# Performance work log

Measured on AMD Instinct MI355X. Metric: run time of the kernel, lower is better.

The kernel has to match this reference:

```python
import jax, jax.numpy as jnp
import numpy as np

HID = 2048
NH = 16
HD = HID // NH  # 128
EPS = 1e-6
BASE = 10000.0


def _rmsnorm(x, w):
    xf = x.astype(jnp.float32)
    y = xf * jax.lax.rsqrt(jnp.mean(xf * xf, axis=-1, keepdims=True) + EPS)
    return y.astype(x.dtype) * w


def _rope_cos_sin(seq_len, dtype):
    inv_freq = 1.0 / (BASE ** (jnp.arange(0, HD, 2, dtype=jnp.float32) / HD))
    t = jnp.arange(seq_len, dtype=jnp.float32)
    freqs = jnp.outer(t, inv_freq)          # [S, HD/2]
    emb = jnp.concatenate([freqs, freqs], axis=-1)  # [S, HD]
    return jnp.cos(emb).astype(dtype), jnp.sin(emb).astype(dtype)


def _rotate_half(x):
    x1, x2 = jnp.split(x, 2, axis=-1)
    return jnp.concatenate([-x2, x1], axis=-1)


def setup_inputs() -> dict:
    key = jax.random.key(0)
    ks = jax.random.split(key, 8)
    B, S = 2, 2048
    s = 0.02
    return {
        "hidden_states": jax.random.normal(ks[0], (B, S, HID), jnp.float32),
        "Wq": jax.random.normal(ks[1], (HID, HID), jnp.float32) * s,
        "Wk": jax.random.normal(ks[2], (HID, HID), jnp.float32) * s,
        "Wv": jax.random.normal(ks[3], (HID, HID), jnp.float32) * s,
        "Wo": jax.random.normal(ks[4], (HID, HID), jnp.float32) * s,
        "w1": jax.random.normal(ks[5], (HID, HID), jnp.float32) * s,
        "w2": jax.random.normal(ks[6], (HID, HID), jnp.float32) * s,
        "w3": jax.random.normal(ks[7], (HID, HID), jnp.float32) * s,
        "ln1_w": jnp.ones((HID,), jnp.float32),
        "ln2_w": jnp.ones((HID,), jnp.float32),
    }


def reference(hidden_states, Wq, Wk, Wv, Wo, w1, w2, w3, ln1_w, ln2_w):
    B, S, _ = hidden_states.shape
    residual = hidden_states
    x = _rmsnorm(hidden_states, ln1_w)

    # projections -> [B, NH, S, HD]
    q = (x @ Wq).reshape(B, S, NH, HD).transpose(0, 2, 1, 3)
    k = (x @ Wk).reshape(B, S, NH, HD).transpose(0, 2, 1, 3)
    v = (x @ Wv).reshape(B, S, NH, HD).transpose(0, 2, 1, 3)

    cos, sin = _rope_cos_sin(S, x.dtype)  # [S, HD]
    cos = cos[None, None]  # broadcast over batch and heads
    sin = sin[None, None]
    q = q * cos + _rotate_half(q) * sin
    k = k * cos + _rotate_half(k) * sin

    scores = jnp.einsum("bhqd,bhkd->bhqk", q, k) / np.sqrt(HD).astype(np.float32)
    # no attention_mask (torch default path). fp32 softmax.
    attn = jax.nn.softmax(scores.astype(jnp.float32), axis=-1).astype(q.dtype)
    ctx = jnp.einsum("bhqk,bhkd->bhqd", attn, v)  # [B, NH, S, HD]
    ctx = ctx.transpose(0, 2, 1, 3).reshape(B, S, HID)
    attn_out = ctx @ Wo

    h = residual + attn_out
    residual = h
    y = _rmsnorm(h, ln2_w)
    mlp = (jax.nn.silu(y @ w1) * (y @ w3)) @ w2
    return residual + mlp
```

## Files before the change

### kernel.cpp

```cpp
#include <hip/hip_runtime.h>

#define HIDN 2048
#define NHEAD 16
#define HD 128
#define SEQ 2048
#define BATCH 2
#define NROWS (BATCH*SEQ)

typedef __bf16 bf16_t;
typedef bf16_t bf16x8 __attribute__((ext_vector_type(8)));
typedef float f32x4 __attribute__((ext_vector_type(4)));

#define AS1 __attribute__((address_space(1)))
#define AS3 __attribute__((address_space(3)))

__device__ __forceinline__ unsigned short f2bf(float x) {
  union { bf16_t b; unsigned short u; } cv; cv.b = (bf16_t)x; return cv.u;
}

#define MFMA16(a,b,c) __builtin_amdgcn_mfma_f32_16x16x32_bf16((a),(b),(c),0,0,0)

__device__ __forceinline__ void gload16(const void* g, void* l) {
  __builtin_amdgcn_global_load_lds((const AS1 void*)g, (AS3 void*)l, 16, 0, 0);
}

__global__ __launch_bounds__(256) void transpose_all_kernel(
    const float* __restrict__ Wq, const float* __restrict__ Wk,
    const float* __restrict__ Wv, const float* __restrict__ Wo,
    const float* __restrict__ w1, const float* __restrict__ w3,
    const float* __restrict__ w2, unsigned short* __restrict__ wblk) {
  const int z = blockIdx.z;
  const float* W; unsigned short* dstb; int tmode = 0, half = 0;
  switch (z) {
    case 0: W = Wq; dstb = wblk;                       tmode = 1; break;
    case 1: W = Wk; dstb = wblk + (size_t)2048 * HIDN; tmode = 1; break;
    case 2: W = Wv; dstb = wblk + (size_t)4096 * HIDN; break;
    case 3: W = Wo; dstb = wblk + (size_t)6144 * HIDN; break;
    case 4: W = w1; dstb = wblk + (size_t)8192 * HIDN; tmode = 2; half = 0; break;
    case 5: W = w3; dstb = wblk + (size_t)8192 * HIDN; tmode = 2; half = 1; break;
    default: W = w2; dstb = wblk + (size_t)12288 * HIDN; break;
  }
  __shared__ float t[64][69];
  const int tid = threadIdx.x;
  const int bn = blockIdx.x * 64, bk = blockIdx.y * 64;
  const int lc = (tid & 15) * 4, lrw = tid >> 4;
#pragma unroll
  for (int i = 0; i < 4; ++i) {
    int k = bk + lrw + i * 16;
    float4 v = *(const float4*)(W + (long)k * HIDN + bn + lc);
    t[lrw + i * 16][lc] = v.x; t[lrw + i * 16][lc + 1] = v.y;
    t[lrw + i * 16][lc + 2] = v.z; t[lrw + i * 16][lc + 3] = v.w;
  }
  __syncthreads();
  const int nl = tid >> 2, k0 = (tid & 3) * 16;
  int n = bn + nl;
  int dst;
  if (tmode == 0) dst = n;
  else if (tmode == 1) { int d = n & 127; dst = (n & ~127) | ((d & 63) << 1) | (d >> 6); }
  else dst = (n >> 4) * 32 + half * 16 + (n & 15);
  unsigned short* orow = dstb + (long)dst * HIDN + bk + k0;
#pragma unroll
  for (int j = 0; j < 16; j += 4) {
    ushort4 o;
    o.x = f2bf(t[k0 + j][nl]);     o.y = f2bf(t[k0 + j + 1][nl]);
    o.z = f2bf(t[k0 + j + 2][nl]); o.w = f2bf(t[k0 + j + 3][nl]);
    *(ushort4*)(orow + j) = o;
  }
}

__global__ void rope_table_kernel(float* __restrict__ cosT, float* __restrict__ sinT) {
  int s = blockIdx.x, d = threadIdx.x;
  float invf = powf(10000.0f, (-2.0f * (float)d) / 128.0f);
  float ang = (float)s * invf;
  cosT[s * 64 + d] = cosf(ang);
  sinT[s * 64 + d] = sinf(ang);
}

__global__ __launch_bounds__(256) void rmsnorm_kernel(
    const float* __restrict__ x, const float* __restrict__ w, unsigned short* __restrict__ out) {
  long row = blockIdx.x;
  const float* xr = x + row * HIDN;
  int c0 = threadIdx.x * 4;
  float4 v0 = *(const float4*)(xr + c0);
  float4 v1 = *(const float4*)(xr + 1024 + c0);
  float s = v0.x*v0.x + v0.y*v0.y + v0.z*v0.z + v0.w*v0.w
          + v1.x*v1.x + v1.y*v1.y + v1.z*v1.z + v1.w*v1.w;
#pragma unroll
  for (int off = 1; off < 64; off <<= 1) s += __shfl_xor(s, off);
  __shared__ float red[4];
  if ((threadIdx.x & 63) == 0) red[threadIdx.x >> 6] = s;
  __syncthreads();
  float tot = red[0] + red[1] + red[2] + red[3];
  float r = 1.0f / sqrtf(tot * (1.0f / (float)HIDN) + 1e-6f);
  float4 w0 = *(const float4*)(w + c0);
  float4 w1 = *(const float4*)(w + 1024 + c0);
  ushort4 o0, o1;
  o0.x = f2bf(v0.x * r * w0.x); o0.y = f2bf(v0.y * r * w0.y);
  o0.z = f2bf(v0.z * r * w0.z); o0.w = f2bf(v0.w * r * w0.w);
  o1.x = f2bf(v1.x * r * w1.x); o1.y = f2bf(v1.y * r * w1.y);
  o1.z = f2bf(v1.z * r * w1.z); o1.w = f2bf(v1.w * r * w1.w);
  *(ushort4*)(out + row * HIDN + c0) = o0;
  *(ushort4*)(out + row * HIDN + 1024 + c0) = o1;
}

template <int MODE>
__global__ __launch_bounds__(512, 2) void gemm256_kernel(
    const unsigned short* __restrict__ A, const unsigned short* __restrict__ Bt,
    int nbx,
    void* __restrict__ p0, void* __restrict__ p1, void* __restrict__ p2,
    const float* __restrict__ cosT, const float* __restrict__ sinT) {
  __shared__ unsigned short L[65536];
  const int tid = threadIdx.x;
  const int wave = tid >> 6, lane = tid & 63;
  const int lr = lane & 15, lkg = lane >> 4;
  const int wr = wave >> 2, wc = wave & 3;
  const int x7 = lr & 7;
  const int nwg = (int)gridDim.x;
  const int bid = (int)blockIdx.x;
  const int wg = (bid & 7) * (nwg >> 3) + (bid >> 3);
  const int bx = wg % nbx, by = wg / nbx;
  const long bm = (long)by * 256, bn = (long)bx * 256;
  const int sslot = (lane & 7) ^ (lane >> 3);
  const unsigned short* Ag = A + (bm + wave * 8 + (lane >> 3)) * HIDN + sslot * 8;
  const unsigned short* Bg = Bt + (bn + wave * 8 + (lane >> 3)) * HIDN + sslot * 8;
  const char* Lc = (const char*)L;
  f32x4 acc[8][4] = {};
  bf16x8 af[2][2], bfr[4][2];

#define STG(b, mat, half, tile)                                                   \
  {                                                                               \
    const unsigned short* gsrc = ((mat) ? Bg : Ag) + ((long)(half) * 128) * HIDN + (long)(tile) * 64; \
    unsigned short* ldst = &L[((4 * (b) + 2 * (mat) + (half)) * 8192) + wave * 8 * 64]; \
    gload16(gsrc, ldst);                                                          \
    gload16(gsrc + (long)64 * HIDN, ldst + 4096);                                 \
  }
#define DSRA(b, q)                                                                \
  { _Pragma("unroll") for (int mm = 0; mm < 2; ++mm) {                            \
      int row128 = ((q) * 2 + mm) * 16 + lr;                                      \
      _Pragma("unroll") for (int ks = 0; ks < 2; ++ks) {                          \
        int s = ks * 4 + lkg;                                                     \
        af[mm][ks] = *(const bf16x8*)(Lc + (4 * (b) + wr) * 16384 + row128 * 128 + ((s ^ x7) << 4)); \
      } } }
#define DSRB(b)                                                                   \
  { _Pragma("unroll") for (int n = 0; n < 4; ++n) {                               \
      int row128 = (wc & 1) * 64 + n * 16 + lr;                                   \
      _Pragma("unroll") for (int ks = 0; ks < 2; ++ks) {                          \
        int s = ks * 4 + lkg;                                                     \
        bfr[n][ks] = *(const bf16x8*)(Lc + (4 * (b) + 2 + (wc >> 1)) * 16384 + row128 * 128 + ((s ^ x7) << 4)); \
      } } }
#define MFMAQ(q)                                                                  \
  { __builtin_amdgcn_s_setprio(1);                                                \
    _Pragma("unroll") for (int mm = 0; mm < 2; ++mm)                              \
      _Pragma("unroll") for (int n = 0; n < 4; ++n) {                             \
        acc[(q) * 2 + mm][n] = MFMA16(af[mm][0], bfr[n][0], acc[(q) * 2 + mm][n]); \
        acc[(q) * 2 + mm][n] = MFMA16(af[mm][1], bfr[n][1], acc[(q) * 2 + mm][n]); \
      }                                                                           \
    __builtin_amdgcn_s_setprio(0); }
#define BARR __builtin_amdgcn_s_barrier()
#define LGK0 { asm volatile("s_waitcnt lgkmcnt(0)" ::: "memory"); __builtin_amdgcn_sched_barrier(0); }

  STG(0, 0, 0, 0); STG(0, 0, 1, 0); STG(0, 1, 0, 0); STG(0, 1, 1, 0);
  STG(1, 1, 0, 1); STG(1, 1, 1, 1); STG(1, 0, 0, 1);
  asm volatile("s_waitcnt vmcnt(6)" ::: "memory");
  __builtin_amdgcn_sched_barrier(0);
  BARR;

  const int NIT = HIDN / 128;
#pragma unroll 1
  for (int i = 0; i < NIT; ++i) {
    const int t2 = 2 * i + 2, t3 = 2 * i + 3;
    const bool nl_ = (i < NIT - 1);
    DSRA(0, 0); DSRB(0);
    STG(1, 0, 1, 2 * i + 1);
    asm volatile("s_waitcnt lgkmcnt(8)" ::: "memory");
    BARR; LGK0; MFMAQ(0); BARR;
    DSRA(0, 1);
    if (nl_) STG(0, 1, 0, t2);
    BARR; LGK0; MFMAQ(1); BARR;
    DSRA(0, 2);
    if (nl_) STG(0, 1, 1, t2);
    BARR; LGK0; MFMAQ(2); BARR;
    DSRA(0, 3);
    BARR; LGK0; MFMAQ(3);
    if (nl_) { asm volatile("s_waitcnt vmcnt(4)" ::: "memory"); }
    else     { asm volatile("s_waitcnt vmcnt(0)" ::: "memory"); }
    __builtin_amdgcn_sched_barrier(0);
    BARR;
    DSRA(1, 0); DSRB(1);
    if (nl_) STG(0, 0, 0, t2);
    asm volatile("s_waitcnt lgkmcnt(8)" ::: "memory");
    BARR; LGK0; MFMAQ(0); BARR;
    DSRA(1, 1);
    if (nl_) { STG(0, 0, 1, t2); STG(1, 1, 0, t3); }
    BARR; LGK0; MFMAQ(1); BARR;
    DSRA(1, 2);
    if (nl_) STG(1, 1, 1, t3);
    BARR; LGK0; MFMAQ(2); BARR;
    DSRA(1, 3);
    if (nl_) STG(1, 0, 0, t3);
    BARR; LGK0; MFMAQ(3);
    if (nl_) { asm volatile("s_waitcnt vmcnt(6)" ::: "memory"); __builtin_amdgcn_sched_barrier(0); }
    BARR;
  }
#undef STG
#undef DSRA
#undef DSRB
#undef MFMAQ
#undef BARR
#undef LGK0

  const int gc0 = (int)bn + wc * 64;
  if (MODE == 1) {
    unsigned short* bout = (unsigned short*)p0;
#pragma unroll
    for (int m = 0; m < 8; ++m) {
      long r0 = bm + wr * 128 + m * 16 + lkg * 4;
#pragma unroll
      for (int n = 0; n < 4; n += 2) {
        int ggrp = (gc0 + n * 16) >> 5;
        long c = (long)ggrp * 16 + lr;
#pragma unroll
        for (int r = 0; r < 4; ++r) {
          float x = acc[m][n][r], g = acc[m][n + 1][r];
          float sv = x / (1.0f + __expf(-x)) * g;
          bout[(r0 + r) * 2048 + c] = f2bf(sv);
        }
      }
    }
  } else {
    int bufid = gc0 >> 11;
    if (bufid == 2) {
      unsigned short* vT = (unsigned short*)p2;
#pragma unroll
      for (int m = 0; m < 8; ++m) {
        long r0 = bm + wr * 128 + m * 16 + lkg * 4;
        long bq = r0 >> 11;
        int s = (int)(r0 & 2047);
#pragma unroll
        for (int n = 0; n < 4; ++n) {
          int wcol = (gc0 + n * 16 + lr) & 2047;
          int hh = wcol >> 7, dd = wcol & 127;
          ushort4 pw;
          pw.x = f2bf(acc[m][n][0]); pw.y = f2bf(acc[m][n][1]);
          pw.z = f2bf(acc[m][n][2]); pw.w = f2bf(acc[m][n][3]);
          *(ushort4*)(vT + ((bq * 16 + hh) * 128 + dd) * (long)SEQ + s) = pw;
        }
      }
    } else {
      unsigned short* dst = (bufid == 0) ? (unsigned short*)p0 : (unsigned short*)p1;
      const float qscale = (bufid == 0) ? 0.12751689f : 1.0f;
#pragma unroll
      for (int m = 0; m < 8; ++m) {
        long r0 = bm + wr * 128 + m * 16 + lkg * 4;
#pragma unroll
        for (int n = 0; n < 4; ++n) {
          int wcol = (gc0 + n * 16 + lr) & 2047;
          int f = wcol & 127, hh = wcol >> 7;
          int j = f >> 1, odd = f & 1;
          int oc = hh * 128 + (odd ? 64 : 0) + j;
#pragma unroll
          for (int r = 0; r < 4; ++r) {
            long row = r0 + r;
            int s = (int)(row & (SEQ - 1));
            float cv = cosT[s * 64 + j], sn = sinT[s * 64 + j];
            float v = acc[m][n][r];
            float o = __shfl_xor(v, 1);
            float res = (odd ? (v * cv + o * sn) : (v * cv - o * sn)) * qscale;
            dst[row * 2048 + oc] = f2bf(res);
          }
        }
      }
    }
  }
}

template <int MODE>
__global__ __launch_bounds__(256) void gemm_kernel(
    const unsigned short* __restrict__ A, const unsigned short* __restrict__ Bt, int N,
    void* __restrict__ p0, const void* __restrict__ p1) {
  __shared__ unsigned short As[128 * 32];
  __shared__ unsigned short Bs[128 * 32];
  const int tid = threadIdx.x;
  const int lane = tid & 63, wave = tid >> 6;
  const int wm = (wave >> 1) * 64, wn = (wave & 1) * 64;
  const int lr = lane & 15, lkg = lane >> 4;
  const long bm = (long)blockIdx.y * 128, bn = (long)blockIdx.x * 128;
  f32x4 acc[4][4] = {};
  const int rA0 = wave * 32 + (lane >> 2);
  const int gs0 = (lane & 3) ^ ((rA0 >> 1) & 3);
  const int gs1 = (lane & 3) ^ (((rA0 + 16) >> 1) & 3);
  const unsigned short* Ag0 = A + (bm + rA0) * HIDN + gs0 * 8;
  const unsigned short* Ag1 = A + (bm + rA0 + 16) * HIDN + gs1 * 8;
  const unsigned short* Bg0 = Bt + (bn + rA0) * HIDN + gs0 * 8;
  const unsigned short* Bg1 = Bt + (bn + rA0 + 16) * HIDN + gs1 * 8;
  unsigned short* lA0 = &As[(wave * 32) * 32];
  unsigned short* lA1 = &As[(wave * 32 + 16) * 32];
  unsigned short* lB0 = &Bs[(wave * 32) * 32];
  unsigned short* lB1 = &Bs[(wave * 32 + 16) * 32];
  for (int k0 = 0; k0 < HIDN; k0 += 32) {
    __syncthreads();
    gload16(Ag0 + k0, lA0);
    gload16(Ag1 + k0, lA1);
    gload16(Bg0 + k0, lB0);
    gload16(Bg1 + k0, lB1);
    __syncthreads();
    bf16x8 af[4], bfr[4];
#pragma unroll
    for (int m = 0; m < 4; ++m) {
      int row = wm + m * 16 + lr;
      af[m] = *(const bf16x8*)((const char*)As + row * 64 + ((lkg ^ ((row >> 1) & 3)) << 4));
    }
#pragma unroll
    for (int n = 0; n < 4; ++n) {
      int row = wn + n * 16 + lr;
      bfr[n] = *(const bf16x8*)((const char*)Bs + row * 64 + ((lkg ^ ((row >> 1) & 3)) << 4));
    }
#pragma unroll
    for (int m = 0; m < 4; ++m)
#pragma unroll
      for (int n = 0; n < 4; ++n) acc[m][n] = MFMA16(af[m], bfr[n], acc[m][n]);
  }
  float* fout = (float*)p0;
  const float* addsrc = (const float*)p1;
#pragma unroll
  for (int m = 0; m < 4; ++m)
#pragma unroll
    for (int n = 0; n < 4; ++n) {
      long r0 = bm + wm + m * 16 + lkg * 4;
      long c = bn + wn + n * 16 + lr;
#pragma unroll
      for (int r = 0; r < 4; ++r) {
        long idx = (r0 + r) * 2048 + c;
        if (MODE == 2) fout[idx] = addsrc[idx] + acc[m][n][r];
        else fout[idx] = fout[idx] + acc[m][n][r];
      }
    }
}

__global__ __launch_bounds__(256, 3) void flash_attn_kernel(
    const unsigned short* __restrict__ Q, const unsigned short* __restrict__ Kb,
    const unsigned short* __restrict__ vT, unsigned short* __restrict__ O) {
  __shared__ unsigned short Ks[64 * 128];
  __shared__ unsigned short Vs[128 * 64];
  __shared__ unsigned short Ps[4][16][72];
  const int bid = (int)blockIdx.x;
  const int wg = (bid & 7) * 128 + (bid >> 3);
  const int qt = wg & 31, h = (wg >> 5) & 15, b = wg >> 9;
  const int tid = threadIdx.x, wave = tid >> 6, lane = tid & 63;
  const int lr = lane & 15, lkg = lane >> 4, lk = lkg * 8;
  const long rowbase = (long)b * SEQ;
  const int qrow0 = qt * 64 + wave * 16;
  bf16x8 aq[4];
#pragma unroll
  for (int ks = 0; ks < 4; ++ks)
    aq[ks] = *(const bf16x8*)(Q + (rowbase + qrow0 + lr) * HIDN + h * HD + ks * 32 + lk);
  const unsigned short* vbase = vT + ((long)(b * 16 + h) * 128) * SEQ;
  const int kr_ = tid >> 4, kc_ = tid & 15;
  const int vd_ = tid >> 3, vc_ = tid & 7;
  int4 kreg[4], vreg[4];
  f32x4 acc[8] = {};
  float m_ = -3.0e38f, l_ = 0.f;

#define GLOADKV(kv0_)                                                              \
  { _Pragma("unroll")                                                              \
    for (int j = 0; j < 4; ++j)                                                    \
      kreg[j] = *(const int4*)(Kb + (rowbase + (kv0_) + kr_ + j * 16) * HIDN + h * HD + kc_ * 8); \
    _Pragma("unroll")                                                              \
    for (int j = 0; j < 4; ++j)                                                    \
      vreg[j] = *(const int4*)(vbase + (long)(vd_ + j * 32) * SEQ + (kv0_) + vc_ * 8); }
#define DSWRITEKV()                                                                \
  { _Pragma("unroll")                                                              \
    for (int j = 0; j < 4; ++j) {                                                  \
      int row = kr_ + j * 16;                                                      \
      *(int4*)((char*)Ks + row * 256 + ((kc_ ^ (row & 15)) << 4)) = kreg[j];       \
    }                                                                              \
    _Pragma("unroll")                                                              \
    for (int j = 0; j < 4; ++j) {                                                  \
      int d = vd_ + j * 32;                                                        \
      *(int4*)((char*)Vs + d * 128 + ((vc_ ^ (d & 7)) << 4)) = vreg[j];            \
    } }

  GLOADKV(0);
  asm volatile("s_waitcnt vmcnt(0)" ::: "memory");
  DSWRITEKV();
  asm volatile("s_waitcnt lgkmcnt(0)" ::: "memory");
  __builtin_amdgcn_sched_barrier(0);
  asm volatile("s_barrier" ::: "memory");

  for (int t = 0; t < SEQ / 64; ++t) {
    if (t + 1 < SEQ / 64) GLOADKV((long)(t + 1) * 64);
    const char* ksb = (const char*)Ks;
    f32x4 sa[4] = {};
#pragma unroll
    for (int n = 0; n < 4; ++n) {
      int row = n * 16 + lr;
#pragma unroll
      for (int ks = 0; ks < 4; ++ks) {
        bf16x8 bk = *(const bf16x8*)(ksb + row * 256 + (((ks * 4 + lkg) ^ (row & 15)) << 4));
        sa[n] = MFMA16(bk, aq[ks], sa[n]);
      }
    }
    float pmax = sa[0][0];
#pragma unroll
    for (int n = 0; n < 4; ++n)
#pragma unroll
      for (int r = 0; r < 4; ++r) pmax = fmaxf(pmax, sa[n][r]);
    pmax = fmaxf(pmax, __shfl_xor(pmax, 16));
    pmax = fmaxf(pmax, __shfl_xor(pmax, 32));
    if (__all(pmax - m_ <= 11.54f)) {
      float psum = 0.f;
#pragma unroll
      for (int n = 0; n < 4; ++n)
#pragma unroll
        for (int r = 0; r < 4; ++r) {
          float p = exp2f(sa[n][r] - m_);
          sa[n][r] = p;
          psum += p;
        }
      psum += __shfl_xor(psum, 16);
      psum += __shfl_xor(psum, 32);
      l_ += psum;
    } else {
      float mnew = fmaxf(m_, pmax);
      float corr = exp2f(m_ - mnew);
      float psum = 0.f;
#pragma unroll
      for (int n = 0; n < 4; ++n)
#pragma unroll
        for (int r = 0; r < 4; ++r) {
          float p = exp2f(sa[n][r] - mnew);
          sa[n][r] = p;
          psum += p;
        }
      psum += __shfl_xor(psum, 16);
      psum += __shfl_xor(psum, 32);
      l_ = l_ * corr + psum;
      m_ = mnew;
      float corr4[4];
#pragma unroll
      for (int r = 0; r < 4; ++r) corr4[r] = __shfl(corr, 4 * lkg + r);
#pragma unroll
      for (int df = 0; df < 8; ++df)
#pragma unroll
        for (int r = 0; r < 4; ++r) acc[df][r] *= corr4[r];
    }
#pragma unroll
    for (int n = 0; n < 4; ++n) {
      ushort4 pw;
      pw.x = f2bf(sa[n][0]); pw.y = f2bf(sa[n][1]);
      pw.z = f2bf(sa[n][2]); pw.w = f2bf(sa[n][3]);
      *(ushort4*)&Ps[wave][lr][n * 16 + 4 * lkg] = pw;
    }
    bf16x8 pa0 = *(const bf16x8*)&Ps[wave][lr][lk];
    bf16x8 pa1 = *(const bf16x8*)&Ps[wave][lr][32 + lk];
    const char* vsb = (const char*)Vs;
#pragma unroll
    for (int df = 0; df < 8; ++df) {
      int row = df * 16 + lr;
      int x7 = row & 7;
      bf16x8 bv0 = *(const bf16x8*)(vsb + row * 128 + ((lkg ^ x7) << 4));
      bf16x8 bv1 = *(const bf16x8*)(vsb + row * 128 + (((4 + lkg) ^ x7) << 4));
      acc[df] = MFMA16(pa0, bv0, acc[df]);
      acc[df] = MFMA16(pa1, bv1, acc[df]);
    }
    asm volatile("s_barrier" ::: "memory");
    if (t + 1 < SEQ / 64) {
      asm volatile("s_waitcnt vmcnt(0)" ::: "memory");
      DSWRITEKV();
      asm volatile("s_waitcnt lgkmcnt(0)" ::: "memory");
      __builtin_amdgcn_sched_barrier(0);
      asm volatile("s_barrier" ::: "memory");
    }
  }
#undef GLOADKV
#undef DSWRITEKV
  float invl = 1.0f / l_;
  float invl4[4];
#pragma unroll
  for (int r = 0; r < 4; ++r) invl4[r] = __shfl(invl, 4 * lkg + r);
#pragma unroll
  for (int r = 0; r < 4; ++r) {
    long orow = rowbase + qrow0 + lkg * 4 + r;
#pragma unroll
    for (int df = 0; df < 8; ++df)
      O[orow * HIDN + h * HD + df * 16 + lr] = f2bf(acc[df][r] * invl4[r]);
  }
}

extern "C" void kernel_launch(void* const* d_in, const int* in_sizes, int n_in,
                              void* d_out, int out_size, void* d_ws, size_t ws_size,
                              hipStream_t stream) {
  const float* hidden = (const float*)d_in[0];
  const float* Wq = (const float*)d_in[1];
  const float* Wk = (const float*)d_in[2];
  const float* Wv = (const float*)d_in[3];
  const float* Wo = (const float*)d_in[4];
  const float* w1 = (const float*)d_in[5];
  const float* w2 = (const float*)d_in[6];
  const float* w3 = (const float*)d_in[7];
  const float* ln1 = (const float*)d_in[8];
  const float* ln2 = (const float*)d_in[9];
  float* out = (float*)d_out;

  char* ws = (char*)d_ws;
  size_t off = 0;
  auto alloc = [&](size_t bytes) -> void* {
    void* p = ws + off;
    off += (bytes + 255) & ~(size_t)255;
    return p;
  };
  unsigned short* wblk = (unsigned short*)alloc((size_t)(2048L * 6 + 2048) * HIDN * 2);
  unsigned short* wQ = wblk;
  unsigned short* wG = wblk + (size_t)8192 * HIDN;
  unsigned short* wO = wblk + (size_t)6144 * HIDN;
  unsigned short* wD = wblk + (size_t)12288 * HIDN;
  unsigned short* xb   = (unsigned short*)alloc((size_t)NROWS * HIDN * 2);
  unsigned short* qb   = (unsigned short*)alloc((size_t)NROWS * HIDN * 2);
  unsigned short* kb   = (unsigned short*)alloc((size_t)NROWS * HIDN * 2);
  unsigned short* vTb  = (unsigned short*)alloc((size_t)NROWS * HIDN * 2);
  unsigned short* ctxb = (unsigned short*)alloc((size_t)NROWS * HIDN * 2);
  float* cosT = (float*)alloc((size_t)SEQ * 64 * 4);
  float* sinT = (float*)alloc((size_t)SEQ * 64 * 4);
  if (off > ws_size) return;

  transpose_all_kernel<<<dim3(HIDN / 64, HIDN / 64, 7), 256, 0, stream>>>(
      Wq, Wk, Wv, Wo, w1, w3, w2, wblk);
  rope_table_kernel<<<SEQ, 64, 0, stream>>>(cosT, sinT);

  rmsnorm_kernel<<<NROWS, 256, 0, stream>>>(hidden, ln1, xb);

  gemm256_kernel<0><<<(6144 / 256) * (NROWS / 256), 512, 0, stream>>>(
      xb, wQ, 6144 / 256, qb, kb, vTb, cosT, sinT);

  flash_attn_kernel<<<(SEQ / 64) * NHEAD * BATCH, 256, 0, stream>>>(qb, kb, vTb, ctxb);

  gemm_kernel<2><<<dim3(2048 / 128, NROWS / 128), 256, 0, stream>>>(
      ctxb, wO, 2048, out, hidden);

  rmsnorm_kernel<<<NROWS, 256, 0, stream>>>(out, ln2, xb);

  gemm256_kernel<1><<<(4096 / 256) * (NROWS / 256), 512, 0, stream>>>(
      xb, wG, 4096 / 256, qb, nullptr, nullptr, nullptr, nullptr);

  gemm_kernel<3><<<dim3(2048 / 128, NROWS / 128), 256, 0, stream>>>(
      qb, wD, 2048, out, nullptr);
}
```

Before: 463.6 us.

## Switch flash attention to 32x32 MFMA with 128-row query tiles

Flash attention now uses 32x32x16 bf16 MFMA and gives each wave 32 query rows, so a block covers 128 queries instead of 64. Each K/V tile loaded into shared memory is reused across twice as many queries, which halves K/V global traffic and LDS staging per query. The softmax reductions and output layout are rewritten for the 32x32 accumulator. In exchange the block count halves (to 512), register pressure rises, and launch bounds drop to two blocks per CU.

```diff
diff --git a/kernel.cpp b/kernel.cpp
--- a/kernel.cpp
+++ b/kernel.cpp
@@ -10,6 +10,7 @@
 typedef __bf16 bf16_t;
 typedef bf16_t bf16x8 __attribute__((ext_vector_type(8)));
 typedef float f32x4 __attribute__((ext_vector_type(4)));
+typedef float f32x16 __attribute__((ext_vector_type(16)));
 
 #define AS1 __attribute__((address_space(1)))
 #define AS3 __attribute__((address_space(3)))
@@ -19,6 +20,7 @@
 }
 
 #define MFMA16(a,b,c) __builtin_amdgcn_mfma_f32_16x16x32_bf16((a),(b),(c),0,0,0)
+#define MFMA32(a,b,c) __builtin_amdgcn_mfma_f32_32x32x16_bf16((a),(b),(c),0,0,0)
 
 __device__ __forceinline__ void gload16(const void* g, void* l) {
   __builtin_amdgcn_global_load_lds((const AS1 void*)g, (AS3 void*)l, 16, 0, 0);
@@ -337,28 +339,28 @@
     }
 }
 
-__global__ __launch_bounds__(256, 3) void flash_attn_kernel(
+__global__ __launch_bounds__(256, 2) void flash_attn_kernel(
     const unsigned short* __restrict__ Q, const unsigned short* __restrict__ Kb,
     const unsigned short* __restrict__ vT, unsigned short* __restrict__ O) {
   __shared__ unsigned short Ks[64 * 128];
   __shared__ unsigned short Vs[128 * 64];
-  __shared__ unsigned short Ps[4][16][72];
+  __shared__ unsigned short Ps[4][32][72];
   const int bid = (int)blockIdx.x;
-  const int wg = (bid & 7) * 128 + (bid >> 3);
-  const int qt = wg & 31, h = (wg >> 5) & 15, b = wg >> 9;
+  const int wg = (bid & 7) * 64 + (bid >> 3);
+  const int qt = wg & 15, h = (wg >> 4) & 15, b = wg >> 8;
   const int tid = threadIdx.x, wave = tid >> 6, lane = tid & 63;
-  const int lr = lane & 15, lkg = lane >> 4, lk = lkg * 8;
+  const int l31 = lane & 31, hi = lane >> 5;
   const long rowbase = (long)b * SEQ;
-  const int qrow0 = qt * 64 + wave * 16;
-  bf16x8 aq[4];
-#pragma unroll
-  for (int ks = 0; ks < 4; ++ks)
-    aq[ks] = *(const bf16x8*)(Q + (rowbase + qrow0 + lr) * HIDN + h * HD + ks * 32 + lk);
+  const int qrow0 = qt * 128 + wave * 32;
+  bf16x8 aq[8];
+#pragma unroll
+  for (int ds = 0; ds < 8; ++ds)
+    aq[ds] = *(const bf16x8*)(Q + (rowbase + qrow0 + l31) * HIDN + h * HD + ds * 16 + 8 * hi);
   const unsigned short* vbase = vT + ((long)(b * 16 + h) * 128) * SEQ;
   const int kr_ = tid >> 4, kc_ = tid & 15;
   const int vd_ = tid >> 3, vc_ = tid & 7;
   int4 kreg[4], vreg[4];
-  f32x4 acc[8] = {};
+  f32x16 acc[4] = {};
   float m_ = -3.0e38f, l_ = 0.f;
 
 #define GLOADKV(kv0_)                                                              \
@@ -390,78 +392,79 @@
   for (int t = 0; t < SEQ / 64; ++t) {
     if (t + 1 < SEQ / 64) GLOADKV((long)(t + 1) * 64);
     const char* ksb = (const char*)Ks;
-    f32x4 sa[4] = {};
-#pragma unroll
-    for (int n = 0; n < 4; ++n) {
-      int row = n * 16 + lr;
-#pragma unroll
-      for (int ks = 0; ks < 4; ++ks) {
-        bf16x8 bk = *(const bf16x8*)(ksb + row * 256 + (((ks * 4 + lkg) ^ (row & 15)) << 4));
-        sa[n] = MFMA16(bk, aq[ks], sa[n]);
-      }
-    }
-    float pmax = sa[0][0];
-#pragma unroll
-    for (int n = 0; n < 4; ++n)
-#pragma unroll
-      for (int r = 0; r < 4; ++r) pmax = fmaxf(pmax, sa[n][r]);
-    pmax = fmaxf(pmax, __shfl_xor(pmax, 16));
-    pmax = fmaxf(pmax, __shfl_xor(pmax, 32));
+    f32x16 sa0 = {}, sa1 = {};
+#pragma unroll
+    for (int ds = 0; ds < 8; ++ds) {
+      int c16 = 2 * ds + hi;
+      int r0 = l31;
+      int r1 = 32 + l31;
+      bf16x8 k0 = *(const bf16x8*)(ksb + r0 * 256 + ((c16 ^ (r0 & 15)) << 4));
+      bf16x8 k1 = *(const bf16x8*)(ksb + r1 * 256 + ((c16 ^ (r1 & 15)) << 4));
+      sa0 = MFMA32(k0, aq[ds], sa0);
+      sa1 = MFMA32(k1, aq[ds], sa1);
+    }
+    float mx[16];
+#pragma unroll
+    for (int i = 0; i < 16; ++i) mx[i] = fmaxf(sa0[i], sa1[i]);
+#pragma unroll
+    for (int s = 8; s > 0; s >>= 1)
+#pragma unroll
+      for (int i = 0; i < 8; ++i) if (i < s) mx[i] = fmaxf(mx[i], mx[i + s]);
+    float pmax = fmaxf(mx[0], __shfl_xor(mx[0], 32));
     if (__all(pmax - m_ <= 11.54f)) {
-      float psum = 0.f;
-#pragma unroll
-      for (int n = 0; n < 4; ++n)
-#pragma unroll
-        for (int r = 0; r < 4; ++r) {
-          float p = exp2f(sa[n][r] - m_);
-          sa[n][r] = p;
-          psum += p;
-        }
-      psum += __shfl_xor(psum, 16);
-      psum += __shfl_xor(psum, 32);
-      l_ += psum;
+      float ps[16];
+#pragma unroll
+      for (int i = 0; i < 16; ++i) {
+        float p0 = exp2f(sa0[i] - m_), p1 = exp2f(sa1[i] - m_);
+        sa0[i] = p0; sa1[i] = p1; ps[i] = p0 + p1;
+      }
+#pragma unroll
+      for (int s = 8; s > 0; s >>= 1)
+#pragma unroll
+        for (int i = 0; i < 8; ++i) if (i < s) ps[i] += ps[i + s];
+      l_ += ps[0] + __shfl_xor(ps[0], 32);
     } else {
       float mnew = fmaxf(m_, pmax);
       float corr = exp2f(m_ - mnew);
-      float psum = 0.f;
-#pragma unroll
-      for (int n = 0; n < 4; ++n)
-#pragma unroll
-        for (int r = 0; r < 4; ++r) {
-          float p = exp2f(sa[n][r] - mnew);
-          sa[n][r] = p;
-          psum += p;
-        }
-      psum += __shfl_xor(psum, 16);
-      psum += __shfl_xor(psum, 32);
-      l_ = l_ * corr + psum;
+      float ps[16];
+#pragma unroll
+      for (int i = 0; i < 16; ++i) {
+        float p0 = exp2f(sa0[i] - mnew), p1 = exp2f(sa1[i] - mnew);
+        sa0[i] = p0; sa1[i] = p1; ps[i] = p0 + p1;
+      }
+#pragma unroll
+      for (int s = 8; s > 0; s >>= 1)
+#pragma unroll
+        for (int i = 0; i < 8; ++i) if (i < s) ps[i] += ps[i + s];
+      l_ = l_ * corr + ps[0] + __shfl_xor(ps[0], 32);
       m_ = mnew;
-      float corr4[4];
-#pragma unroll
-      for (int r = 0; r < 4; ++r) corr4[r] = __shfl(corr, 4 * lkg + r);
-#pragma unroll
-      for (int df = 0; df < 8; ++df)
-#pragma unroll
-        for (int r = 0; r < 4; ++r) acc[df][r] *= corr4[r];
-    }
-#pragma unroll
-    for (int n = 0; n < 4; ++n) {
-      ushort4 pw;
-      pw.x = f2bf(sa[n][0]); pw.y = f2bf(sa[n][1]);
-      pw.z = f2bf(sa[n][2]); pw.w = f2bf(sa[n][3]);
-      *(ushort4*)&Ps[wave][lr][n * 16 + 4 * lkg] = pw;
-    }
-    bf16x8 pa0 = *(const bf16x8*)&Ps[wave][lr][lk];
-    bf16x8 pa1 = *(const bf16x8*)&Ps[wave][lr][32 + lk];
+#pragma unroll
+      for (int db = 0; db < 4; ++db) acc[db] *= corr;
+    }
+#pragma unroll
+    for (int g = 0; g < 4; ++g) {
+      ushort4 w0, w1;
+      w0.x = f2bf(sa0[4 * g]);     w0.y = f2bf(sa0[4 * g + 1]);
+      w0.z = f2bf(sa0[4 * g + 2]); w0.w = f2bf(sa0[4 * g + 3]);
+      w1.x = f2bf(sa1[4 * g]);     w1.y = f2bf(sa1[4 * g + 1]);
+      w1.z = f2bf(sa1[4 * g + 2]); w1.w = f2bf(sa1[4 * g + 3]);
+      *(ushort4*)&Ps[wave][l31][8 * g + 4 * hi]      = w0;
+      *(ushort4*)&Ps[wave][l31][32 + 8 * g + 4 * hi] = w1;
+    }
+    bf16x8 pfrag[4];
+#pragma unroll
+    for (int ks = 0; ks < 4; ++ks)
+      pfrag[ks] = *(const bf16x8*)&Ps[wave][l31][ks * 16 + 8 * hi];
     const char* vsb = (const char*)Vs;
 #pragma unroll
-    for (int df = 0; df < 8; ++df) {
-      int row = df * 16 + lr;
-      int x7 = row & 7;
-      bf16x8 bv0 = *(const bf16x8*)(vsb + row * 128 + ((lkg ^ x7) << 4));
-      bf16x8 bv1 = *(const bf16x8*)(vsb + row * 128 + (((4 + lkg) ^ x7) << 4));
-      acc[df] = MFMA16(pa0, bv0, acc[df]);
-      acc[df] = MFMA16(pa1, bv1, acc[df]);
+    for (int db = 0; db < 4; ++db) {
+      int d = db * 32 + l31;
+      int x7 = d & 7;
+#pragma unroll
+      for (int ks = 0; ks < 4; ++ks) {
+        bf16x8 vf = *(const bf16x8*)(vsb + d * 128 + (((2 * ks + hi) ^ x7) << 4));
+        acc[db] = MFMA32(vf, pfrag[ks], acc[db]);
+      }
     }
     asm volatile("s_barrier" ::: "memory");
     if (t + 1 < SEQ / 64) {
@@ -475,16 +478,14 @@
 #undef GLOADKV
 #undef DSWRITEKV
   float invl = 1.0f / l_;
-  float invl4[4];
-#pragma unroll
-  for (int r = 0; r < 4; ++r) invl4[r] = __shfl(invl, 4 * lkg + r);
-#pragma unroll
-  for (int r = 0; r < 4; ++r) {
-    long orow = rowbase + qrow0 + lkg * 4 + r;
-#pragma unroll
-    for (int df = 0; df < 8; ++df)
-      O[orow * HIDN + h * HD + df * 16 + lr] = f2bf(acc[df][r] * invl4[r]);
-  }
+  unsigned short* orow = O + (rowbase + qrow0 + l31) * HIDN + h * HD;
+#pragma unroll
+  for (int db = 0; db < 4; ++db)
+#pragma unroll
+    for (int i = 0; i < 16; ++i) {
+      int d = db * 32 + (i & 3) + 8 * (i >> 2) + 4 * hi;
+      orow[d] = f2bf(acc[db][i] * invl);
+    }
 }
 
 extern "C" void kernel_launch(void* const* d_in, const int* in_sizes, int n_in,
@@ -532,7 +533,7 @@
   gemm256_kernel<0><<<(6144 / 256) * (NROWS / 256), 512, 0, stream>>>(
       xb, wQ, 6144 / 256, qb, kb, vTb, cosT, sinT);
 
-  flash_attn_kernel<<<(SEQ / 64) * NHEAD * BATCH, 256, 0, stream>>>(qb, kb, vTb, ctxb);
+  flash_attn_kernel<<<(SEQ / 128) * NHEAD * BATCH, 256, 0, stream>>>(qb, kb, vTb, ctxb);
 
   gemm_kernel<2><<<dim3(2048 / 128, NROWS / 128), 256, 0, stream>>>(
       ctxb, wO, 2048, out, hidden);
```

Result: slower. 523.0 us (+12.8%).

## Process 32 query rows per wave in flash attention to reuse K/V tiles

Applied to the files above, without the earlier changes.

Each wave now handles two 16-row query subtiles (128 queries per block instead of 64), sharing each K and V LDS fragment read across both sets of MFMAs. This halves the number of blocks and the total K/V global loads and LDS writes per query, raising MFMA work per LDS read. It doubles accumulator and softmax register state, so launch bounds drop from 3 to 2 blocks per CU, reducing occupancy and the grid to 512 blocks.

```diff
diff --git a/kernel.cpp b/kernel.cpp
--- a/kernel.cpp
+++ b/kernel.cpp
@@ -337,29 +337,31 @@
     }
 }
 
-__global__ __launch_bounds__(256, 3) void flash_attn_kernel(
+__global__ __launch_bounds__(256, 2) void flash_attn_kernel(
     const unsigned short* __restrict__ Q, const unsigned short* __restrict__ Kb,
     const unsigned short* __restrict__ vT, unsigned short* __restrict__ O) {
   __shared__ unsigned short Ks[64 * 128];
   __shared__ unsigned short Vs[128 * 64];
-  __shared__ unsigned short Ps[4][16][72];
+  __shared__ unsigned short Ps[4][32][72];
   const int bid = (int)blockIdx.x;
-  const int wg = (bid & 7) * 128 + (bid >> 3);
-  const int qt = wg & 31, h = (wg >> 5) & 15, b = wg >> 9;
+  const int wg = (bid & 7) * 64 + (bid >> 3);
+  const int qt = wg & 15, h = (wg >> 4) & 15, b = wg >> 8;
   const int tid = threadIdx.x, wave = tid >> 6, lane = tid & 63;
   const int lr = lane & 15, lkg = lane >> 4, lk = lkg * 8;
   const long rowbase = (long)b * SEQ;
-  const int qrow0 = qt * 64 + wave * 16;
-  bf16x8 aq[4];
-#pragma unroll
-  for (int ks = 0; ks < 4; ++ks)
-    aq[ks] = *(const bf16x8*)(Q + (rowbase + qrow0 + lr) * HIDN + h * HD + ks * 32 + lk);
+  const int qrow0 = qt * 128 + wave * 32;
+  bf16x8 aqA[4], aqB[4];
+#pragma unroll
+  for (int ks = 0; ks < 4; ++ks) {
+    aqA[ks] = *(const bf16x8*)(Q + (rowbase + qrow0 + lr) * HIDN + h * HD + ks * 32 + lk);
+    aqB[ks] = *(const bf16x8*)(Q + (rowbase + qrow0 + 16 + lr) * HIDN + h * HD + ks * 32 + lk);
+  }
   const unsigned short* vbase = vT + ((long)(b * 16 + h) * 128) * SEQ;
   const int kr_ = tid >> 4, kc_ = tid & 15;
   const int vd_ = tid >> 3, vc_ = tid & 7;
   int4 kreg[4], vreg[4];
-  f32x4 acc[8] = {};
-  float m_ = -3.0e38f, l_ = 0.f;
+  f32x4 accA[8] = {}, accB[8] = {};
+  float mA = -3.0e38f, lA_ = 0.f, mB = -3.0e38f, lB_ = 0.f;
 
 #define GLOADKV(kv0_)                                                              \
   { _Pragma("unroll")                                                              \
@@ -379,6 +381,42 @@
       int d = vd_ + j * 32;                                                        \
       *(int4*)((char*)Vs + d * 128 + ((vc_ ^ (d & 7)) << 4)) = vreg[j];            \
     } }
+#define SOFTMAX(sa, m_, l_, acc)                                                   \
+  {                                                                                \
+    float pmax = sa[0][0];                                                         \
+    _Pragma("unroll") for (int n = 0; n < 4; ++n)                                  \
+      _Pragma("unroll") for (int r = 0; r < 4; ++r) pmax = fmaxf(pmax, sa[n][r]);  \
+    pmax = fmaxf(pmax, __shfl_xor(pmax, 16));                                      \
+    pmax = fmaxf(pmax, __shfl_xor(pmax, 32));                                      \
+    if (__all(pmax - m_ <= 11.54f)) {                                              \
+      float psum = 0.f;                                                            \
+      _Pragma("unroll") for (int n = 0; n < 4; ++n)                                \
+        _Pragma("unroll") for (int r = 0; r < 4; ++r) {                            \
+          float p = exp2f(sa[n][r] - m_);                                          \
+          sa[n][r] = p; psum += p;                                                 \
+        }                                                                          \
+      psum += __shfl_xor(psum, 16);                                                \
+      psum += __shfl_xor(psum, 32);                                                \
+      l_ += psum;                                                                  \
+    } else {                                                                       \
+      float mnew = fmaxf(m_, pmax);                                                \
+      float corr = exp2f(m_ - mnew);                                               \
+      float psum = 0.f;                                                            \
+      _Pragma("unroll") for (int n = 0; n < 4; ++n)                                \
+        _Pragma("unroll") for (int r = 0; r < 4; ++r) {                            \
+          float p = exp2f(sa[n][r] - mnew);                                        \
+          sa[n][r] = p; psum += p;                                                 \
+        }                                                                          \
+      psum += __shfl_xor(psum, 16);                                                \
+      psum += __shfl_xor(psum, 32);                                                \
+      l_ = l_ * corr + psum;                                                       \
+      m_ = mnew;                                                                   \
+      float corr4[4];                                                              \
+      _Pragma("unroll") for (int r = 0; r < 4; ++r) corr4[r] = __shfl(corr, 4 * lkg + r); \
+      _Pragma("unroll") for (int df = 0; df < 8; ++df)                             \
+        _Pragma("unroll") for (int r = 0; r < 4; ++r) acc[df][r] *= corr4[r];      \
+    }                                                                              \
+  }
 
   GLOADKV(0);
   asm volatile("s_waitcnt vmcnt(0)" ::: "memory");
@@ -390,69 +428,33 @@
   for (int t = 0; t < SEQ / 64; ++t) {
     if (t + 1 < SEQ / 64) GLOADKV((long)(t + 1) * 64);
     const char* ksb = (const char*)Ks;
-    f32x4 sa[4] = {};
+    f32x4 saA[4] = {}, saB[4] = {};
 #pragma unroll
     for (int n = 0; n < 4; ++n) {
       int row = n * 16 + lr;
 #pragma unroll
       for (int ks = 0; ks < 4; ++ks) {
         bf16x8 bk = *(const bf16x8*)(ksb + row * 256 + (((ks * 4 + lkg) ^ (row & 15)) << 4));
-        sa[n] = MFMA16(bk, aq[ks], sa[n]);
+        saA[n] = MFMA16(bk, aqA[ks], saA[n]);
+        saB[n] = MFMA16(bk, aqB[ks], saB[n]);
       }
     }
-    float pmax = sa[0][0];
-#pragma unroll
-    for (int n = 0; n < 4; ++n)
-#pragma unroll
-      for (int r = 0; r < 4; ++r) pmax = fmaxf(pmax, sa[n][r]);
-    pmax = fmaxf(pmax, __shfl_xor(pmax, 16));
-    pmax = fmaxf(pmax, __shfl_xor(pmax, 32));
-    if (__all(pmax - m_ <= 11.54f)) {
-      float psum = 0.f;
-#pragma unroll
-      for (int n = 0; n < 4; ++n)
-#pragma unroll
-        for (int r = 0; r < 4; ++r) {
-          float p = exp2f(sa[n][r] - m_);
-          sa[n][r] = p;
-          psum += p;
-        }
-      psum += __shfl_xor(psum, 16);
-      psum += __shfl_xor(psum, 32);
-      l_ += psum;
-    } else {
-      float mnew = fmaxf(m_, pmax);
-      float corr = exp2f(m_ - mnew);
-      float psum = 0.f;
-#pragma unroll
-      for (int n = 0; n < 4; ++n)
-#pragma unroll
-        for (int r = 0; r < 4; ++r) {
-          float p = exp2f(sa[n][r] - mnew);
-          sa[n][r] = p;
-          psum += p;
-        }
-      psum += __shfl_xor(psum, 16);
-      psum += __shfl_xor(psum, 32);
-      l_ = l_ * corr + psum;
-      m_ = mnew;
-      float corr4[4];
-#pragma unroll
-      for (int r = 0; r < 4; ++r) corr4[r] = __shfl(corr, 4 * lkg + r);
-#pragma unroll
-      for (int df = 0; df < 8; ++df)
-#pragma unroll
-        for (int r = 0; r < 4; ++r) acc[df][r] *= corr4[r];
-    }
+    SOFTMAX(saA, mA, lA_, accA);
+    SOFTMAX(saB, mB, lB_, accB);
 #pragma unroll
     for (int n = 0; n < 4; ++n) {
-      ushort4 pw;
-      pw.x = f2bf(sa[n][0]); pw.y = f2bf(sa[n][1]);
-      pw.z = f2bf(sa[n][2]); pw.w = f2bf(sa[n][3]);
-      *(ushort4*)&Ps[wave][lr][n * 16 + 4 * lkg] = pw;
-    }
-    bf16x8 pa0 = *(const bf16x8*)&Ps[wave][lr][lk];
-    bf16x8 pa1 = *(const bf16x8*)&Ps[wave][lr][32 + lk];
+      ushort4 pwA, pwB;
+      pwA.x = f2bf(saA[n][0]); pwA.y = f2bf(saA[n][1]);
+      pwA.z = f2bf(saA[n][2]); pwA.w = f2bf(saA[n][3]);
+      pwB.x = f2bf(saB[n][0]); pwB.y = f2bf(saB[n][1]);
+      pwB.z = f2bf(saB[n][2]); pwB.w = f2bf(saB[n][3]);
+      *(ushort4*)&Ps[wave][lr][n * 16 + 4 * lkg]      = pwA;
+      *(ushort4*)&Ps[wave][16 + lr][n * 16 + 4 * lkg] = pwB;
+    }
+    bf16x8 paA0 = *(const bf16x8*)&Ps[wave][lr][lk];
+    bf16x8 paA1 = *(const bf16x8*)&Ps[wave][lr][32 + lk];
+    bf16x8 paB0 = *(const bf16x8*)&Ps[wave][16 + lr][lk];
+    bf16x8 paB1 = *(const bf16x8*)&Ps[wave][16 + lr][32 + lk];
     const char* vsb = (const char*)Vs;
 #pragma unroll
     for (int df = 0; df < 8; ++df) {
@@ -460,8 +462,10 @@
       int x7 = row & 7;
       bf16x8 bv0 = *(const bf16x8*)(vsb + row * 128 + ((lkg ^ x7) << 4));
       bf16x8 bv1 = *(const bf16x8*)(vsb + row * 128 + (((4 + lkg) ^ x7) << 4));
-      acc[df] = MFMA16(pa0, bv0, acc[df]);
-      acc[df] = MFMA16(pa1, bv1, acc[df]);
+      accA[df] = MFMA16(paA0, bv0, accA[df]);
+      accA[df] = MFMA16(paA1, bv1, accA[df]);
+      accB[df] = MFMA16(paB0, bv0, accB[df]);
+      accB[df] = MFMA16(paB1, bv1, accB[df]);
     }
     asm volatile("s_barrier" ::: "memory");
     if (t + 1 < SEQ / 64) {
@@ -474,16 +478,23 @@
   }
 #undef GLOADKV
 #undef DSWRITEKV
-  float invl = 1.0f / l_;
-  float invl4[4];
-#pragma unroll
-  for (int r = 0; r < 4; ++r) invl4[r] = __shfl(invl, 4 * lkg + r);
+#undef SOFTMAX
+  float invlA = 1.0f / lA_, invlB = 1.0f / lB_;
+  float invA4[4], invB4[4];
 #pragma unroll
   for (int r = 0; r < 4; ++r) {
-    long orow = rowbase + qrow0 + lkg * 4 + r;
-#pragma unroll
-    for (int df = 0; df < 8; ++df)
-      O[orow * HIDN + h * HD + df * 16 + lr] = f2bf(acc[df][r] * invl4[r]);
+    invA4[r] = __shfl(invlA, 4 * lkg + r);
+    invB4[r] = __shfl(invlB, 4 * lkg + r);
+  }
+#pragma unroll
+  for (int r = 0; r < 4; ++r) {
+    long orowA = rowbase + qrow0 + lkg * 4 + r;
+    long orowB = rowbase + qrow0 + 16 + lkg * 4 + r;
+#pragma unroll
+    for (int df = 0; df < 8; ++df) {
+      O[orowA * HIDN + h * HD + df * 16 + lr] = f2bf(accA[df][r] * invA4[r]);
+      O[orowB * HIDN + h * HD + df * 16 + lr] = f2bf(accB[df][r] * invB4[r]);
+    }
   }
 }
 
@@ -532,7 +543,7 @@
   gemm256_kernel<0><<<(6144 / 256) * (NROWS / 256), 512, 0, stream>>>(
       xb, wQ, 6144 / 256, qb, kb, vTb, cosT, sinT);
 
-  flash_attn_kernel<<<(SEQ / 64) * NHEAD * BATCH, 256, 0, stream>>>(qb, kb, vTb, ctxb);
+  flash_attn_kernel<<<(SEQ / 128) * NHEAD * BATCH, 256, 0, stream>>>(qb, kb, vTb, ctxb);
 
   gemm_kernel<2><<<dim3(2048 / 128, NROWS / 128), 256, 0, stream>>>(
       ctxb, wO, 2048, out, hidden);
```

Measured after the change: 514.2 us. +10.9%, slower.
